# Kernel tuning notes

Hardware: AMD Instinct MI355X
Metric: run time of the kernel (lower is better)

## Reference

```python
import jax, jax.numpy as jnp
import numpy as np

SIGMA_DATA = 16.0
ALPHA_BOND = 1.0


def safe_norm(x, axis=-1):
    # L2 norm with zero (sub)gradient at 0, matching torch.norm's behavior
    sq = jnp.sum(x * x, axis=axis)
    n = jnp.sqrt(jnp.where(sq > 0, sq, 1.0))
    return jnp.where(sq > 0, n, 0.0)


def weighted_rigid_align(x_l, xGT_l, w_l):
    # Aligns x_l onto xGT_l's frame (Kabsch with weights); output is detached.
    wm = w_l[..., None]                                   # [B,N,1]
    denom = jnp.sum(wm, axis=1, keepdims=True)
    mu = jnp.sum(wm * x_l, axis=1, keepdims=True) / denom
    muGT = jnp.sum(wm * xGT_l, axis=1, keepdims=True) / denom
    xc = x_l - mu
    xGTc = xGT_l - muGT
    # M = (w * xGT_c)^T @ x_c  -> [B,3,3]
    M = jnp.einsum('bni,bnj->bij', wm * xGTc, xc)
    U, S, Vh = jnp.linalg.svd(M)
    R = U @ Vh
    det = jnp.linalg.det(R)
    Fm = jnp.array([[1.0, 0.0, 0.0], [0.0, 1.0, 0.0], [0.0, 0.0, -1.0]], dtype=R.dtype)
    Rfix = jnp.einsum('bij,jk,bkl->bil', U, Fm, Vh)
    R = jnp.where(det[:, None, None] < 0, Rfix, R)
    xalign = xc @ jnp.swapaxes(R, -1, -2) + muGT
    return jax.lax.stop_gradient(xalign)


def diffusion_loss(xpred_l, xGT_l, ht, w_l):
    # Align ground truth onto prediction (note arg order in original forward)
    xGT_aligned = weighted_rigid_align(xGT_l, xpred_l, w_l)
    loss = jnp.sum(safe_norm(xpred_l - xGT_aligned) * w_l) / jnp.sum(w_l)
    if ALPHA_BOND > 0:
        w_pair = w_l[:, :, None] * w_l[:, None, :]                 # [B,N,N]
        d_pred = safe_norm(xpred_l[:, :, None] - xpred_l[:, None]) # [B,N,N]
        d_gt = safe_norm(xGT_l[:, :, None] - xGT_l[:, None])       # [B,N,N]
        L_bond = w_pair * (d_pred - d_gt) ** 2
        loss = loss + ALPHA_BOND * jnp.sum(L_bond) / jnp.sum(w_pair)
    return (ht ** 2 + SIGMA_DATA ** 2) / (ht + SIGMA_DATA) ** 2 * loss


def setup_inputs() -> dict:
    key = jax.random.key(0)
    k1, k2, k3, k4 = jax.random.split(key, 4)
    B, N = 4, 2048
    xpred_l = jax.random.normal(k1, (B, N, 3), dtype=jnp.float32) * 10.0
    xGT_l = jax.random.normal(k2, (B, N, 3), dtype=jnp.float32) * 10.0
    ht = jax.random.uniform(k3, (B,), dtype=jnp.float32, minval=0.1, maxval=4.0)
    w_l = jax.random.uniform(k4, (B, N), dtype=jnp.float32, minval=0.1, maxval=1.0)
    return {"xpred_l": xpred_l, "xGT_l": xGT_l, "ht": ht, "w_l": w_l}


def reference(xpred_l, xGT_l, ht, w_l):
    return diffusion_loss(xpred_l, xGT_l, ht, w_l)
```

## Files before the change

kernel.cpp:

```cpp
#include <hip/hip_runtime.h>
#include <math.h>


#define RT 256
#define CT 64
#define MAXB 8

__global__ __launch_bounds__(RT, 4)
void k_main(const float* __restrict__ pred, const float* __restrict__ gt,
            const float* __restrict__ ht, const float* __restrict__ w,
            float* __restrict__ out, double* __restrict__ ws,
            int N, int B, unsigned total) {
    const int b    = blockIdx.z;
    const int bx   = blockIdx.x;
    const int r0   = bx * RT;
    const int c0   = blockIdx.y * CT;
    const int tid  = threadIdx.x;
    const int lane = tid & 63, wave = tid >> 6;
    const int GX   = gridDim.x;
    const unsigned linear = (blockIdx.z * gridDim.y + blockIdx.y) * GX + blockIdx.x;

    double*   statsSlot = ws;
    double*   bondSlot  = ws + (size_t)B * GX * 16;
    unsigned* cnt       = (unsigned*)(bondSlot + total);

    const float* p  = pred + (size_t)b * N * 3;
    const float* g  = gt   + (size_t)b * N * 3;
    const float* wb = w    + (size_t)b * N;

    __shared__ float4 sp4[CT], sg4[CT];
    __shared__ double shred[4][16];

    const int  n      = r0 + tid;
    const bool row_ok = (n < N);
    float px=0.f,py=0.f,pz=0.f,gx=0.f,gy=0.f,gz=0.f,wn=0.f;
    if (row_ok) {
        px = p[3*n]; py = p[3*n+1]; pz = p[3*n+2];
        gx = g[3*n]; gy = g[3*n+1]; gz = g[3*n+2];
        wn = wb[n];
    }

    const bool bond_active = (c0 + CT > r0 + 1) && (c0 < N);
    float bond_f = 0.0f;
    if (bond_active) {
        for (int i = tid; i < CT; i += RT) {
            int m = c0 + i;
            float4 a = make_float4(0.f,0.f,0.f,0.f), c = a;
            if (m < N) {
                a = make_float4(p[3*m], p[3*m+1], p[3*m+2], wb[m]);
                c = make_float4(g[3*m], g[3*m+1], g[3*m+2], 0.f);
            }
            sp4[i] = a; sg4[i] = c;
        }
        __syncthreads();
        if (row_ok) {
            const int cc = min(CT, N - c0);
            if (c0 >= r0 + RT) {
                #pragma unroll 4
                for (int i = 0; i < cc; i++) {
                    float4 cp = sp4[i], cg = sg4[i];
                    float dxp=px-cp.x, dyp=py-cp.y, dzp=pz-cp.z;
                    float dxg=gx-cg.x, dyg=gy-cg.y, dzg=gz-cg.z;
                    float dp = sqrtf(dxp*dxp+dyp*dyp+dzp*dzp);
                    float dg = sqrtf(dxg*dxg+dyg*dyg+dzg*dzg);
                    float dd = dp - dg;
                    bond_f += (wn*cp.w)*(dd*dd);
                }
            } else if (n < c0 + cc - 1) {
                #pragma unroll 4
                for (int i = 0; i < cc; i++) {
                    float4 cp = sp4[i], cg = sg4[i];
                    float dxp=px-cp.x, dyp=py-cp.y, dzp=pz-cp.z;
                    float dxg=gx-cg.x, dyg=gy-cg.y, dzg=gz-cg.z;
                    float dp = sqrtf(dxp*dxp+dyp*dyp+dzp*dzp);
                    float dg = sqrtf(dxg*dxg+dyg*dyg+dzg*dzg);
                    float dd = dp - dg;
                    float t  = (wn*cp.w)*(dd*dd);
                    bond_f += (c0 + i > n) ? t : 0.0f;
                }
            }
        }
    }
    bond_f *= 2.0f;

    if (blockIdx.y == 0) {
        double wd=wn, pxd=px,pyd=py,pzd=pz, gxd=gx,gyd=gy,gzd=gz;
        double st[16] = {wd, wd*pxd, wd*pyd, wd*pzd, wd*gxd, wd*gyd, wd*gzd,
                         wd*pxd*gxd, wd*pxd*gyd, wd*pxd*gzd,
                         wd*pyd*gxd, wd*pyd*gyd, wd*pyd*gzd,
                         wd*pzd*gxd, wd*pzd*gyd, wd*pzd*gzd};
        #pragma unroll
        for (int off = 32; off > 0; off >>= 1) {
            #pragma unroll
            for (int k = 0; k < 16; k++) st[k] += __shfl_down(st[k], off, 64);
        }
        if (lane == 0) {
            #pragma unroll
            for (int k = 0; k < 16; k++) shred[wave][k] = st[k];
        }
        __syncthreads();
        if (tid < 16)
            __hip_atomic_store(&statsSlot[((size_t)b*GX + bx)*16 + tid],
                               shred[0][tid]+shred[1][tid]+shred[2][tid]+shred[3][tid],
                               __ATOMIC_RELAXED, __HIP_MEMORY_SCOPE_AGENT);
        __syncthreads();
    }

    double bd = (double)bond_f;
    #pragma unroll
    for (int off = 32; off > 0; off >>= 1) bd += __shfl_down(bd, off, 64);
    if (lane == 0) shred[wave][0] = bd;
    __syncthreads();
    if (tid == 0)
        __hip_atomic_store(&bondSlot[linear],
                           shred[0][0]+shred[1][0]+shred[2][0]+shred[3][0],
                           __ATOMIC_RELAXED, __HIP_MEMORY_SCOPE_AGENT);

    __shared__ unsigned s_old;
    __syncthreads();
    if (tid == 0) s_old = __hip_atomic_fetch_add(cnt, 1u, __ATOMIC_RELAXED,
                                                 __HIP_MEMORY_SCOPE_AGENT);
    __syncthreads();
    if (s_old != total - 1u) return;

    __shared__ double sstat[MAXB][16];
    __shared__ float  Rf[MAXB][15];
    __shared__ double Wd[MAXB];
    __shared__ double s_bond, s_loss;

    if (tid < B * 16) {
        int bb = tid >> 4, k = tid & 15;
        double acc = 0.0;
        for (int j = 0; j < GX; j++)
            acc += __hip_atomic_load(&statsSlot[((size_t)bb*GX + j)*16 + k],
                                     __ATOMIC_RELAXED, __HIP_MEMORY_SCOPE_AGENT);
        sstat[bb][k] = acc;
    }

    double bsum = 0.0;
    for (unsigned i = tid; i < total; i += RT)
        bsum += __hip_atomic_load(&bondSlot[i], __ATOMIC_RELAXED,
                                  __HIP_MEMORY_SCOPE_AGENT);
    #pragma unroll
    for (int off = 32; off > 0; off >>= 1) bsum += __shfl_down(bsum, off, 64);
    if (lane == 0) shred[wave][1] = bsum;
    __syncthreads();
    if (tid == 0) s_bond = shred[0][1]+shred[1][1]+shred[2][1]+shred[3][1];

    if (tid < B) {
        const double* s = sstat[tid];
        double W = s[0];
        double mup[3] = { s[1]/W, s[2]/W, s[3]/W };
        double mug[3] = { s[4]/W, s[5]/W, s[6]/W };
        double M[3][3];
        for (int i = 0; i < 3; i++)
            for (int j = 0; j < 3; j++)
                M[i][j] = s[7 + i*3 + j] - W * mup[i] * mug[j];
        double A[3][3];
        for (int i = 0; i < 3; i++)
            for (int j = 0; j < 3; j++) {
                double t = 0.0;
                for (int k = 0; k < 3; k++) t += M[k][i] * M[k][j];
                A[i][j] = t;
            }
        double V[3][3] = {{1,0,0},{0,1,0},{0,0,1}};
        for (int sweep = 0; sweep < 5; sweep++) {
            for (int pq = 0; pq < 3; pq++) {
                int pp_ = (pq == 2) ? 1 : 0;
                int qq_ = (pq == 0) ? 1 : 2;
                double apq = A[pp_][qq_];
                if (fabs(apq) < 1e-300) continue;
                double app = A[pp_][pp_], aqq = A[qq_][qq_];
                double theta = (aqq - app) / (2.0 * apq);
                double t = copysign(1.0, theta) / (fabs(theta) + sqrt(theta*theta + 1.0));
                double cj = 1.0 / sqrt(t*t + 1.0), sn = t * cj;
                A[pp_][pp_] = app - t * apq;
                A[qq_][qq_] = aqq + t * apq;
                A[pp_][qq_] = A[qq_][pp_] = 0.0;
                int r = 3 - pp_ - qq_;
                double arp = A[r][pp_], arq = A[r][qq_];
                A[r][pp_] = A[pp_][r] = cj*arp - sn*arq;
                A[r][qq_] = A[qq_][r] = sn*arp + cj*arq;
                for (int rr = 0; rr < 3; rr++) {
                    double vp = V[rr][pp_], vq = V[rr][qq_];
                    V[rr][pp_] = cj*vp - sn*vq;
                    V[rr][qq_] = sn*vp + cj*vq;
                }
            }
        }
        double d[3] = { A[0][0], A[1][1], A[2][2] };
        int idx[3] = {0, 1, 2};
        for (int i = 0; i < 2; i++)
            for (int j = i + 1; j < 3; j++)
                if (d[idx[j]] > d[idx[i]]) { int tt = idx[i]; idx[i] = idx[j]; idx[j] = tt; }
        double u[3][3], v[3][3];
        for (int i = 0; i < 3; i++) {
            int c_ = idx[i];
            double sv = sqrt(fmax(d[c_], 0.0));
            double inv = (sv > 1e-12) ? 1.0 / sv : 0.0;
            for (int r = 0; r < 3; r++) v[i][r] = V[r][c_];
            for (int r = 0; r < 3; r++) {
                double t = 0.0;
                for (int k = 0; k < 3; k++) t += M[r][k] * v[i][k];
                u[i][r] = t * inv;
            }
        }
        double detM = M[0][0]*(M[1][1]*M[2][2] - M[1][2]*M[2][1])
                    - M[0][1]*(M[1][0]*M[2][2] - M[1][2]*M[2][0])
                    + M[0][2]*(M[1][0]*M[2][1] - M[1][1]*M[2][0]);
        double sg2 = (detM < 0.0) ? -1.0 : 1.0;
        for (int r = 0; r < 3; r++)
            for (int cc2 = 0; cc2 < 3; cc2++)
                Rf[tid][r*3+cc2] = (float)(u[0][r]*v[0][cc2] + u[1][r]*v[1][cc2]
                                           + sg2 * u[2][r]*v[2][cc2]);
        for (int i = 0; i < 3; i++) Rf[tid][9 + i]  = (float)mup[i];
        for (int i = 0; i < 3; i++) Rf[tid][12 + i] = (float)mug[i];
        Wd[tid] = W;
    }
    __syncthreads();

    double al = 0.0;
    for (int bb = 0; bb < B; bb++) {
        float R0=Rf[bb][0], R1=Rf[bb][1], R2=Rf[bb][2];
        float R3=Rf[bb][3], R4=Rf[bb][4], R5=Rf[bb][5];
        float R6=Rf[bb][6], R7=Rf[bb][7], R8=Rf[bb][8];
        float mp0=Rf[bb][9],  mp1=Rf[bb][10], mp2=Rf[bb][11];
        float mg0=Rf[bb][12], mg1=Rf[bb][13], mg2=Rf[bb][14];
        const float* pp  = pred + (size_t)bb * N * 3;
        const float* gg  = gt   + (size_t)bb * N * 3;
        const float* wwb = w    + (size_t)bb * N;
        for (int nn = tid; nn < N; nn += RT) {
            float x0 = gg[3*nn]-mg0, x1 = gg[3*nn+1]-mg1, x2 = gg[3*nn+2]-mg2;
            float ax = fmaf(R0,x0, fmaf(R1,x1, fmaf(R2,x2, mp0)));
            float ay = fmaf(R3,x0, fmaf(R4,x1, fmaf(R5,x2, mp1)));
            float az = fmaf(R6,x0, fmaf(R7,x1, fmaf(R8,x2, mp2)));
            float ex = pp[3*nn]-ax, ey = pp[3*nn+1]-ay, ez = pp[3*nn+2]-az;
            float sq = ex*ex + ey*ey + ez*ez;
            al += (double)(wwb[nn] * sqrtf(sq));
        }
    }
    #pragma unroll
    for (int off = 32; off > 0; off >>= 1) al += __shfl_down(al, off, 64);
    if (lane == 0) shred[wave][2] = al;
    __syncthreads();
    if (tid == 0) {
        double at = shred[0][2]+shred[1][2]+shred[2][2]+shred[3][2];
        double tw = 0.0, twp = 0.0;
        for (int i = 0; i < B; i++) { double W = Wd[i]; tw += W; twp += W*W; }
        s_loss = at / tw + s_bond / twp;
    }
    __syncthreads();
    if (tid < B) {
        double h = (double)ht[tid];
        out[tid] = (float)(((h*h + 256.0) / ((h + 16.0)*(h + 16.0))) * s_loss);
    }
}

extern "C" void kernel_launch(void* const* d_in, const int* in_sizes, int n_in,
                              void* d_out, int out_size, void* d_ws, size_t ws_size,
                              hipStream_t stream) {
    const float* pred = (const float*)d_in[0];
    const float* gt   = (const float*)d_in[1];
    const float* ht   = (const float*)d_in[2];
    const float* w    = (const float*)d_in[3];
    int B = in_sizes[2];
    int N = in_sizes[3] / B;
    double* ws = (double*)d_ws;
    float* out = (float*)d_out;

    int gx = (N + RT - 1) / RT;
    int gy = (N + CT - 1) / CT;
    unsigned total = (unsigned)(gx * gy * B);
    size_t cnt_off = ((size_t)B * gx * 16 + total) * sizeof(double);

    hipMemsetAsync((char*)d_ws + cnt_off, 0, sizeof(unsigned), stream);
    k_main<<<dim3(gx, gy, B), dim3(RT), 0, stream>>>(pred, gt, ht, w, out, ws, N, B, total);
}
```

Baseline: 100.7 us.

## Double column tile, use hierarchical completion counters, run Jacobi SVD in fp32

Column tile width CT doubles from 64 to 128, which halves the number of blocks and the per-block partial slots to reduce. The single global completion counter is replaced by per-group counters, one per 32 blocks and padded apart, plus a top-level counter, to reduce atomic contention. The last block now runs the 3x3 Jacobi eigen-solve in fp32 on a max-normalised matrix while keeping the determinant sign in double. The fp32 solve risks accuracy loss, and a larger tile may lower occupancy or load balance.

Result: slower. 106.1 us (+5.3%).

```diff
diff --git a/kernel.cpp b/kernel.cpp
--- a/kernel.cpp
+++ b/kernel.cpp
@@ -3,14 +3,14 @@
 
 
 #define RT 256
-#define CT 64
+#define CT 128
 #define MAXB 8
 
 __global__ __launch_bounds__(RT, 4)
 void k_main(const float* __restrict__ pred, const float* __restrict__ gt,
             const float* __restrict__ ht, const float* __restrict__ w,
             float* __restrict__ out, double* __restrict__ ws,
-            int N, int B, unsigned total) {
+            int N, int B, unsigned total, unsigned ngroups) {
     const int b    = blockIdx.z;
     const int bx   = blockIdx.x;
     const int r0   = bx * RT;
@@ -118,10 +118,19 @@
 
     __shared__ unsigned s_old;
     __syncthreads();
-    if (tid == 0) s_old = __hip_atomic_fetch_add(cnt, 1u, __ATOMIC_RELAXED,
-                                                 __HIP_MEMORY_SCOPE_AGENT);
-    __syncthreads();
-    if (s_old != total - 1u) return;
+    if (tid == 0) {
+        unsigned grp   = linear >> 5;
+        unsigned gsize = min(32u, total - (grp << 5));
+        unsigned og = __hip_atomic_fetch_add(&cnt[grp * 32], 1u,
+                                             __ATOMIC_RELAXED, __HIP_MEMORY_SCOPE_AGENT);
+        unsigned ov = 0xFFFFFFFFu;
+        if (og == gsize - 1u)
+            ov = __hip_atomic_fetch_add(&cnt[ngroups * 32], 1u,
+                                        __ATOMIC_RELAXED, __HIP_MEMORY_SCOPE_AGENT);
+        s_old = ov;
+    }
+    __syncthreads();
+    if (s_old != ngroups - 1u) return;
 
     __shared__ double sstat[MAXB][16];
     __shared__ float  Rf[MAXB][15];
@@ -150,71 +159,80 @@
     if (tid < B) {
         const double* s = sstat[tid];
         double W = s[0];
-        double mup[3] = { s[1]/W, s[2]/W, s[3]/W };
-        double mug[3] = { s[4]/W, s[5]/W, s[6]/W };
-        double M[3][3];
-        for (int i = 0; i < 3; i++)
-            for (int j = 0; j < 3; j++)
-                M[i][j] = s[7 + i*3 + j] - W * mup[i] * mug[j];
-        double A[3][3];
+        double mupd[3] = { s[1]/W, s[2]/W, s[3]/W };
+        double mugd[3] = { s[4]/W, s[5]/W, s[6]/W };
+        double Md[3][3];
+        double mmax = 0.0;
         for (int i = 0; i < 3; i++)
             for (int j = 0; j < 3; j++) {
-                double t = 0.0;
+                Md[i][j] = s[7 + i*3 + j] - W * mupd[i] * mugd[j];
+                mmax = fmax(mmax, fabs(Md[i][j]));
+            }
+        double detM = Md[0][0]*(Md[1][1]*Md[2][2] - Md[1][2]*Md[2][1])
+                    - Md[0][1]*(Md[1][0]*Md[2][2] - Md[1][2]*Md[2][0])
+                    + Md[0][2]*(Md[1][0]*Md[2][1] - Md[1][1]*Md[2][0]);
+        float sg2 = (detM < 0.0) ? -1.0f : 1.0f;
+
+        float M[3][3];
+        float inv_mmax = (mmax > 0.0) ? (float)(1.0 / mmax) : 0.0f;
+        for (int i = 0; i < 3; i++)
+            for (int j = 0; j < 3; j++) M[i][j] = (float)Md[i][j] * inv_mmax;
+
+        float A[3][3];
+        for (int i = 0; i < 3; i++)
+            for (int j = 0; j < 3; j++) {
+                float t = 0.0f;
                 for (int k = 0; k < 3; k++) t += M[k][i] * M[k][j];
                 A[i][j] = t;
             }
-        double V[3][3] = {{1,0,0},{0,1,0},{0,0,1}};
-        for (int sweep = 0; sweep < 5; sweep++) {
+        float V[3][3] = {{1,0,0},{0,1,0},{0,0,1}};
+        for (int sweep = 0; sweep < 6; sweep++) {
             for (int pq = 0; pq < 3; pq++) {
                 int pp_ = (pq == 2) ? 1 : 0;
                 int qq_ = (pq == 0) ? 1 : 2;
-                double apq = A[pp_][qq_];
-                if (fabs(apq) < 1e-300) continue;
-                double app = A[pp_][pp_], aqq = A[qq_][qq_];
-                double theta = (aqq - app) / (2.0 * apq);
-                double t = copysign(1.0, theta) / (fabs(theta) + sqrt(theta*theta + 1.0));
-                double cj = 1.0 / sqrt(t*t + 1.0), sn = t * cj;
+                float apq = A[pp_][qq_];
+                if (fabsf(apq) < 1e-30f) continue;
+                float app = A[pp_][pp_], aqq = A[qq_][qq_];
+                float theta = (aqq - app) / (2.0f * apq);
+                float t = copysignf(1.0f, theta) / (fabsf(theta) + sqrtf(theta*theta + 1.0f));
+                float cj = 1.0f / sqrtf(t*t + 1.0f), sn = t * cj;
                 A[pp_][pp_] = app - t * apq;
                 A[qq_][qq_] = aqq + t * apq;
-                A[pp_][qq_] = A[qq_][pp_] = 0.0;
+                A[pp_][qq_] = A[qq_][pp_] = 0.0f;
                 int r = 3 - pp_ - qq_;
-                double arp = A[r][pp_], arq = A[r][qq_];
+                float arp = A[r][pp_], arq = A[r][qq_];
                 A[r][pp_] = A[pp_][r] = cj*arp - sn*arq;
                 A[r][qq_] = A[qq_][r] = sn*arp + cj*arq;
                 for (int rr = 0; rr < 3; rr++) {
-                    double vp = V[rr][pp_], vq = V[rr][qq_];
+                    float vp = V[rr][pp_], vq = V[rr][qq_];
                     V[rr][pp_] = cj*vp - sn*vq;
                     V[rr][qq_] = sn*vp + cj*vq;
                 }
             }
         }
-        double d[3] = { A[0][0], A[1][1], A[2][2] };
+        float d[3] = { A[0][0], A[1][1], A[2][2] };
         int idx[3] = {0, 1, 2};
         for (int i = 0; i < 2; i++)
             for (int j = i + 1; j < 3; j++)
                 if (d[idx[j]] > d[idx[i]]) { int tt = idx[i]; idx[i] = idx[j]; idx[j] = tt; }
-        double u[3][3], v[3][3];
+        float u[3][3], v[3][3];
         for (int i = 0; i < 3; i++) {
             int c_ = idx[i];
-            double sv = sqrt(fmax(d[c_], 0.0));
-            double inv = (sv > 1e-12) ? 1.0 / sv : 0.0;
+            float sv = sqrtf(fmaxf(d[c_], 0.0f));
+            float inv = (sv > 1e-7f) ? 1.0f / sv : 0.0f;
             for (int r = 0; r < 3; r++) v[i][r] = V[r][c_];
             for (int r = 0; r < 3; r++) {
-                double t = 0.0;
+                float t = 0.0f;
                 for (int k = 0; k < 3; k++) t += M[r][k] * v[i][k];
                 u[i][r] = t * inv;
             }
         }
-        double detM = M[0][0]*(M[1][1]*M[2][2] - M[1][2]*M[2][1])
-                    - M[0][1]*(M[1][0]*M[2][2] - M[1][2]*M[2][0])
-                    + M[0][2]*(M[1][0]*M[2][1] - M[1][1]*M[2][0]);
-        double sg2 = (detM < 0.0) ? -1.0 : 1.0;
         for (int r = 0; r < 3; r++)
             for (int cc2 = 0; cc2 < 3; cc2++)
-                Rf[tid][r*3+cc2] = (float)(u[0][r]*v[0][cc2] + u[1][r]*v[1][cc2]
-                                           + sg2 * u[2][r]*v[2][cc2]);
-        for (int i = 0; i < 3; i++) Rf[tid][9 + i]  = (float)mup[i];
-        for (int i = 0; i < 3; i++) Rf[tid][12 + i] = (float)mug[i];
+                Rf[tid][r*3+cc2] = u[0][r]*v[0][cc2] + u[1][r]*v[1][cc2]
+                                 + sg2 * u[2][r]*v[2][cc2];
+        for (int i = 0; i < 3; i++) Rf[tid][9 + i]  = (float)mupd[i];
+        for (int i = 0; i < 3; i++) Rf[tid][12 + i] = (float)mugd[i];
         Wd[tid] = W;
     }
     __syncthreads();
@@ -270,9 +288,12 @@
 
     int gx = (N + RT - 1) / RT;
     int gy = (N + CT - 1) / CT;
-    unsigned total = (unsigned)(gx * gy * B);
-    size_t cnt_off = ((size_t)B * gx * 16 + total) * sizeof(double);
-
-    hipMemsetAsync((char*)d_ws + cnt_off, 0, sizeof(unsigned), stream);
-    k_main<<<dim3(gx, gy, B), dim3(RT), 0, stream>>>(pred, gt, ht, w, out, ws, N, B, total);
+    unsigned total   = (unsigned)(gx * gy * B);
+    unsigned ngroups = (total + 31u) >> 5;
+    size_t cnt_off   = ((size_t)B * gx * 16 + total) * sizeof(double);
+    size_t cnt_bytes = ((size_t)ngroups * 32 + 1) * sizeof(unsigned);
+
+    hipMemsetAsync((char*)d_ws + cnt_off, 0, cnt_bytes, stream);
+    k_main<<<dim3(gx, gy, B), dim3(RT), 0, stream>>>(pred, gt, ht, w, out, ws,
+                                                     N, B, total, ngroups);
 }
```
